# Kernel optimization log

Hardware: AMD Instinct MI355X
Metric: run time of the kernel (lower is better)

The kernel has to match this reference:

```python
import jax, jax.numpy as jnp
import numpy as np

TEMPERATURE = 8.0  # sqrt(head_dim=64)


def setup_inputs() -> dict:
    key = jax.random.key(0)
    ks = jax.random.split(key, 6)
    B, H, S, D = 8, 8, 1024, 64
    shp = (B, H, S, D)
    names = ["q_r", "q_i", "k_r", "k_i", "v_r", "v_i"]
    return {n: jax.random.normal(k, shp, dtype=jnp.float32) for n, k in zip(names, ks)}


def _mag_minmax_norm(attn):
    """cvnn.MagMinMaxNorm(dim=-1): min-max normalize the magnitude along the
    last axis while preserving phase: x * (|x| - min) / ((max - min) * |x|)."""
    mag = jnp.abs(attn)                              # [B,H,Sq,Sk] real
    mn = jnp.min(mag, axis=-1, keepdims=True)
    mx = jnp.max(mag, axis=-1, keepdims=True)
    return attn * ((mag - mn) / ((mx - mn) * mag))


def reference(q_r, q_i, k_r, k_i, v_r, v_i):
    q = jax.lax.complex(q_r, q_i)
    k = jax.lax.complex(k_r, k_i)
    v = jax.lax.complex(v_r, v_i)
    # complex QK^T with temperature scaling
    attn = jnp.einsum("bhqd,bhkd->bhqk", q / TEMPERATURE, k)
    attn = _mag_minmax_norm(attn)
    # dropout is identity at inference (eval mode)
    out = jnp.einsum("bhqk,bhkd->bhqd", attn, v)
    # return real/imag stacked: [2, B, H, S, D]
    return jnp.stack([out.real, out.imag])
```

## Files before the change

### kernel.cpp

```cpp
#include <hip/hip_runtime.h>
#include <math.h>

typedef unsigned short ushort_t;
typedef __attribute__((ext_vector_type(8))) short short8;
typedef __attribute__((ext_vector_type(4))) float f32x4;
typedef __attribute__((ext_vector_type(4))) int int4v;

constexpr int S = 1024, D = 64, BH = 64;
constexpr int HALF = BH * S * D;
constexpr int KROW = 72;
constexpr int VROW = 72;
constexpr int TILE_USH = 2 * 32 * KROW + 64 * VROW;
constexpr int TILE_B = TILE_USH * 2;
constexpr size_t WS_NEED = (size_t)BH * 32 * TILE_B;

#define MFMA16(a, b, c) __builtin_amdgcn_mfma_f32_16x16x32_bf16(a, b, c, 0, 0, 0)

__device__ __forceinline__ ushort_t f2bf(float f) {
  unsigned u = __float_as_uint(f);
  u += 0x7fff + ((u >> 16) & 1);
  return (ushort_t)(u >> 16);
}

__device__ __forceinline__ int4v pack8(float4 a, float4 b) {
  int4v r;
  r.x = (unsigned)f2bf(a.x) | ((unsigned)f2bf(a.y) << 16);
  r.y = (unsigned)f2bf(a.z) | ((unsigned)f2bf(a.w) << 16);
  r.z = (unsigned)f2bf(b.x) | ((unsigned)f2bf(b.y) << 16);
  r.w = (unsigned)f2bf(b.z) | ((unsigned)f2bf(b.w) << 16);
  return r;
}

#if defined(__has_builtin)
#if __has_builtin(__builtin_amdgcn_cvt_pk_bf16_f32)
#define HAS_CVT_PK_BF16 1
typedef __attribute__((ext_vector_type(2))) __bf16 bf16x2_t;
__device__ __forceinline__ unsigned cvtpk(float a, float b) {
  bf16x2_t v = __builtin_amdgcn_cvt_pk_bf16_f32(a, b);
  unsigned u;
  __builtin_memcpy(&u, &v, 4);
  return u;
}
#endif
#endif
#ifndef HAS_CVT_PK_BF16
#define HAS_CVT_PK_BF16 0
__device__ __forceinline__ unsigned cvtpk(float a, float b) {
  return (unsigned)f2bf(a) | ((unsigned)f2bf(b) << 16);
}
#endif

__device__ __forceinline__ short8 twist(short8 v) {
  int4v u;
  __builtin_memcpy(&u, &v, 16);
  int4v w;
  w.x = (int)((((unsigned)u.x >> 16) | ((unsigned)u.x << 16)) ^ 0x8000u);
  w.y = (int)((((unsigned)u.y >> 16) | ((unsigned)u.y << 16)) ^ 0x8000u);
  w.z = (int)((((unsigned)u.z >> 16) | ((unsigned)u.z << 16)) ^ 0x8000u);
  w.w = (int)((((unsigned)u.w >> 16) | ((unsigned)u.w << 16)) ^ 0x8000u);
  short8 r;
  __builtin_memcpy(&r, &w, 16);
  return r;
}

__global__ __launch_bounds__(256)
void prepass_kernel(const float* __restrict__ kr, const float* __restrict__ ki,
                    const float* __restrict__ vr, const float* __restrict__ vi,
                    ushort_t* __restrict__ ws) {
  __shared__ float svr[32 * 65], svi[32 * 65];
  const int t = threadIdx.x;
  const int tile = blockIdx.x;
  const size_t gbase = (size_t)tile * (32 * D);
  ushort_t* wst = ws + (size_t)tile * TILE_USH;
  const int k = t >> 3, d0 = (t & 7) * 8;
  const int dT = t >> 2, k0 = (t & 3) * 8;

  {
    float4 a = *(const float4*)(kr + gbase + k * D + d0);
    float4 b = *(const float4*)(kr + gbase + k * D + d0 + 4);
    *(int4v*)(wst + k * KROW + d0) = pack8(a, b);
  }
  {
    float4 a = *(const float4*)(ki + gbase + k * D + d0);
    float4 b = *(const float4*)(ki + gbase + k * D + d0 + 4);
    *(int4v*)(wst + 2304 + k * KROW + d0) = pack8(a, b);
  }
  {
    float4 a = *(const float4*)(vr + gbase + k * D + d0);
    float4 b = *(const float4*)(vr + gbase + k * D + d0 + 4);
    *(float4*)&svr[k * 65 + d0] = a;
    *(float4*)&svr[k * 65 + d0 + 4] = b;
    float4 c = *(const float4*)(vi + gbase + k * D + d0);
    float4 d = *(const float4*)(vi + gbase + k * D + d0 + 4);
    *(float4*)&svi[k * 65 + d0] = c;
    *(float4*)&svi[k * 65 + d0 + 4] = d;
  }
  __syncthreads();
  {
    unsigned dws[8];
#pragma unroll
    for (int j = 0; j < 8; ++j) {
      int s = k0 + j;
      dws[j] = cvtpk(svr[s * 65 + dT], -svi[s * 65 + dT]);
    }
    ushort_t* dst = wst + 4608 + dT * VROW + 2 * k0;
    *(int4v*)dst = *(int4v*)&dws[0];
    *(int4v*)(dst + 8) = *(int4v*)&dws[4];
  }
}

__global__ __launch_bounds__(256, 2)
void cvattn_mfma(const float* __restrict__ gq_r, const float* __restrict__ gq_i,
                 const ushort_t* __restrict__ ws, float* __restrict__ gout) {
  __shared__ __attribute__((aligned(16))) char smem[55296];
  ushort_t* sB = (ushort_t*)smem;
  const int t = threadIdx.x;
  const int lane = t & 63, wave = t >> 6;
  const int m = lane & 15, quad = lane >> 4;
  const int qt = blockIdx.x, bh = blockIdx.y;
  const size_t base = (size_t)bh * (S * D);

  unsigned* pwu = (unsigned*)(smem + 18432) + wave * 2304;

  short8 fQr[2][2], fQi[2][2];
#pragma unroll
  for (int h = 0; h < 2; ++h) {
    const int row = qt * 128 + h * 64 + wave * 16 + m;
#pragma unroll
    for (int dc = 0; dc < 2; ++dc) {
      const int d = dc * 32 + quad * 8;
      const float* pr = gq_r + base + (size_t)row * D + d;
      const float* pi = gq_i + base + (size_t)row * D + d;
      int4v vr_ = pack8(*(const float4*)pr, *(const float4*)(pr + 4));
      int4v vi_ = pack8(*(const float4*)pi, *(const float4*)(pi + 4));
      __builtin_memcpy(&fQr[h][dc], &vr_, 16);
      __builtin_memcpy(&fQi[h][dc], &vi_, 16);
    }
  }

  f32x4 aAr[2][4] = {}, aAi[2][4] = {}, aUr[2][4] = {}, aUi[2][4] = {};
  float mn4[2][4], mx4[2][4];
#pragma unroll
  for (int h = 0; h < 2; ++h)
#pragma unroll
    for (int r = 0; r < 4; ++r) { mn4[h][r] = 1e30f; mx4[h][r] = 0.f; }

  const ushort_t* wsrc = ws + (size_t)bh * 32 * TILE_USH;

  int4v pre[5];
#pragma unroll
  for (int i = 0; i < 5; ++i) {
    int idx = i * 256 + t;
    if (idx < TILE_B / 16) pre[i] = *(const int4v*)(wsrc + idx * 8);
  }

  for (int kb = 0; kb < 32; ++kb) {
    __syncthreads();
#pragma unroll
    for (int i = 0; i < 5; ++i) {
      int idx = i * 256 + t;
      if (idx < TILE_B / 16) *(int4v*)(smem + idx * 16) = pre[i];
    }
    if (kb + 1 < 32) {
      const ushort_t* g = wsrc + (size_t)(kb + 1) * TILE_USH;
#pragma unroll
      for (int i = 0; i < 5; ++i) {
        int idx = i * 256 + t;
        if (idx < TILE_B / 16) pre[i] = *(const int4v*)(g + idx * 8);
      }
    }
    __syncthreads();

#pragma unroll
    for (int ks = 0; ks < 2; ++ks) {
      const int krow = ks * 16 + m;
      short8 fKr0 = *(const short8*)&sB[krow * KROW + quad * 8];
      short8 fKr1 = *(const short8*)&sB[krow * KROW + 32 + quad * 8];
      short8 fKi0 = *(const short8*)&sB[2304 + krow * KROW + quad * 8];
      short8 fKi1 = *(const short8*)&sB[2304 + krow * KROW + 32 + quad * 8];
      short8 fKn0 = fKi0 ^ (short)0x8000;
      short8 fKn1 = fKi1 ^ (short)0x8000;
#pragma unroll
      for (int h = 0; h < 2; ++h) {
        f32x4 cSr = {}, cSi = {};
        cSr = MFMA16(fQr[h][0], fKr0, cSr);
        cSr = MFMA16(fQr[h][1], fKr1, cSr);
        cSr = MFMA16(fQi[h][0], fKn0, cSr);
        cSr = MFMA16(fQi[h][1], fKn1, cSr);
        cSi = MFMA16(fQr[h][0], fKi0, cSi);
        cSi = MFMA16(fQr[h][1], fKi1, cSi);
        cSi = MFMA16(fQi[h][0], fKr0, cSi);
        cSi = MFMA16(fQi[h][1], fKr1, cSi);
#pragma unroll
        for (int r = 0; r < 4; ++r) {
          float sr = cSr[r], si = cSi[r];
          float t2 = sr * sr + si * si;
          float rq = __builtin_amdgcn_rsqf(t2);
          mn4[h][r] = fminf(mn4[h][r], t2);
          mx4[h][r] = fmaxf(mx4[h][r], t2);
          const int dwo = h * 1152 + (quad * 4 + r) * 36 + ks * 16 + m;
          pwu[dwo] = cvtpk(sr, si);
          pwu[576 + dwo] = cvtpk(sr * rq, si * rq);
        }
      }
    }

    short8 fP0[2], fP1[2], fU0[2], fU1[2];
#pragma unroll
    for (int h = 0; h < 2; ++h) {
      const int bo = h * 1152 + m * 36 + quad * 4;
      fP0[h] = *(const short8*)&pwu[bo];
      fP1[h] = *(const short8*)&pwu[bo + 16];
      fU0[h] = *(const short8*)&pwu[576 + bo];
      fU1[h] = *(const short8*)&pwu[576 + bo + 16];
    }
#pragma unroll
    for (int dt = 0; dt < 4; ++dt) {
      const unsigned* vrow = (const unsigned*)sB + 2304 + (dt * 16 + m) * 36 + quad * 4;
      short8 vre0 = *(const short8*)vrow;
      short8 vre1 = *(const short8*)(vrow + 16);
      short8 vim0 = twist(vre0);
      short8 vim1 = twist(vre1);
#pragma unroll
      for (int h = 0; h < 2; ++h) {
        aAr[h][dt] = MFMA16(fP0[h], vre0, aAr[h][dt]);
        aAr[h][dt] = MFMA16(fP1[h], vre1, aAr[h][dt]);
        aAi[h][dt] = MFMA16(fP0[h], vim0, aAi[h][dt]);
        aAi[h][dt] = MFMA16(fP1[h], vim1, aAi[h][dt]);
        aUr[h][dt] = MFMA16(fU0[h], vre0, aUr[h][dt]);
        aUr[h][dt] = MFMA16(fU1[h], vre1, aUr[h][dt]);
        aUi[h][dt] = MFMA16(fU0[h], vim0, aUi[h][dt]);
        aUi[h][dt] = MFMA16(fU1[h], vim1, aUi[h][dt]);
      }
    }
  }

#pragma unroll
  for (int h = 0; h < 2; ++h) {
    float inv[4];
#pragma unroll
    for (int r = 0; r < 4; ++r) {
#pragma unroll
      for (int mask = 1; mask < 16; mask <<= 1) {
        mn4[h][r] = fminf(mn4[h][r], __shfl_xor(mn4[h][r], mask, 64));
        mx4[h][r] = fmaxf(mx4[h][r], __shfl_xor(mx4[h][r], mask, 64));
      }
      mn4[h][r] = sqrtf(mn4[h][r]);
      mx4[h][r] = sqrtf(mx4[h][r]);
      inv[r] = 1.0f / (mx4[h][r] - mn4[h][r]);
    }
    const int qbase = qt * 128 + h * 64 + wave * 16 + quad * 4;
#pragma unroll
    for (int dt = 0; dt < 4; ++dt) {
      const int d = dt * 16 + m;
#pragma unroll
      for (int r = 0; r < 4; ++r) {
        size_t o = base + (size_t)(qbase + r) * D + d;
        gout[o] = (aAr[h][dt][r] - mn4[h][r] * aUr[h][dt][r]) * inv[r];
        gout[HALF + o] = (aAi[h][dt][r] - mn4[h][r] * aUi[h][dt][r]) * inv[r];
      }
    }
  }
}

constexpr int QT = 32, KT = 32;
constexpr int DP = D + 4;
constexpr int KP = KT + 1;

#define CDOT4(SR, SI, AR, AI, BR, BI)                              \
  SR += AR.x*BR.x + AR.y*BR.y + AR.z*BR.z + AR.w*BR.w              \
      - AI.x*BI.x - AI.y*BI.y - AI.z*BI.z - AI.w*BI.w;             \
  SI += AR.x*BI.x + AR.y*BI.y + AR.z*BI.z + AR.w*BI.w              \
      + AI.x*BR.x + AI.y*BR.y + AI.z*BR.z + AI.w*BR.w;

__global__ __launch_bounds__(256, 2)
void cvattn_fallback(const float* __restrict__ gq_r, const float* __restrict__ gq_i,
                     const float* __restrict__ gk_r, const float* __restrict__ gk_i,
                     const float* __restrict__ gv_r, const float* __restrict__ gv_i,
                     float* __restrict__ gout) {
  __shared__ float qs_r[QT][DP], qs_i[QT][DP];
  __shared__ float ks_r[KT][DP], ks_i[KT][DP];
  __shared__ float vs_r[KT][DP], vs_i[KT][DP];
  __shared__ float sc_r[QT][KP], sc_i[QT][KP], sc_m[QT][KP];
  const int t = threadIdx.x;
  const int qt2 = blockIdx.x, bh = blockIdx.y;
  const size_t base = (size_t)bh * (S * D);
  {
    const float* qr_p = gq_r + base + (size_t)qt2 * QT * D;
    const float* qi_p = gq_i + base + (size_t)qt2 * QT * D;
#pragma unroll
    for (int i = 0; i < 2; ++i) {
      int e = (t + i * 256) * 4;
      int row = e >> 6, col = e & 63;
      *(float4*)&qs_r[row][col] = *(const float4*)(qr_p + e);
      *(float4*)&qs_i[row][col] = *(const float4*)(qi_p + e);
    }
  }
  const int q0 = (t >> 4) * 2, k0 = (t & 15) * 2;
  const int rB = t >> 3, dc = (t & 7) * 8;
  float Ar[8] = {}, Ai[8] = {}, Ur[8] = {}, Ui[8] = {};
  float mn = 3.4e38f, mx = 0.0f;
  for (int kb = 0; kb < S / KT; ++kb) {
    __syncthreads();
    {
      const float* kr_p = gk_r + base + (size_t)kb * KT * D;
      const float* ki_p = gk_i + base + (size_t)kb * KT * D;
      const float* vr_p = gv_r + base + (size_t)kb * KT * D;
      const float* vi_p = gv_i + base + (size_t)kb * KT * D;
#pragma unroll
      for (int i = 0; i < 2; ++i) {
        int e = (t + i * 256) * 4;
        int row = e >> 6, col = e & 63;
        *(float4*)&ks_r[row][col] = *(const float4*)(kr_p + e);
        *(float4*)&ks_i[row][col] = *(const float4*)(ki_p + e);
        *(float4*)&vs_r[row][col] = *(const float4*)(vr_p + e);
        *(float4*)&vs_i[row][col] = *(const float4*)(vi_p + e);
      }
    }
    __syncthreads();
    {
      float s00r=0.f,s00i=0.f,s01r=0.f,s01i=0.f;
      float s10r=0.f,s10i=0.f,s11r=0.f,s11i=0.f;
#pragma unroll
      for (int d = 0; d < D; d += 4) {
        float4 a0r = *(const float4*)&qs_r[q0  ][d];
        float4 a0i = *(const float4*)&qs_i[q0  ][d];
        float4 a1r = *(const float4*)&qs_r[q0+1][d];
        float4 a1i = *(const float4*)&qs_i[q0+1][d];
        float4 b0r = *(const float4*)&ks_r[k0  ][d];
        float4 b0i = *(const float4*)&ks_i[k0  ][d];
        float4 b1r = *(const float4*)&ks_r[k0+1][d];
        float4 b1i = *(const float4*)&ks_i[k0+1][d];
        CDOT4(s00r, s00i, a0r, a0i, b0r, b0i);
        CDOT4(s01r, s01i, a0r, a0i, b1r, b1i);
        CDOT4(s10r, s10i, a1r, a1i, b0r, b0i);
        CDOT4(s11r, s11i, a1r, a1i, b1r, b1i);
      }
      s00r *= 0.125f; s00i *= 0.125f; s01r *= 0.125f; s01i *= 0.125f;
      s10r *= 0.125f; s10i *= 0.125f; s11r *= 0.125f; s11i *= 0.125f;
      sc_r[q0  ][k0  ] = s00r; sc_i[q0  ][k0  ] = s00i;
      sc_m[q0  ][k0  ] = sqrtf(s00r*s00r + s00i*s00i);
      sc_r[q0  ][k0+1] = s01r; sc_i[q0  ][k0+1] = s01i;
      sc_m[q0  ][k0+1] = sqrtf(s01r*s01r + s01i*s01i);
      sc_r[q0+1][k0  ] = s10r; sc_i[q0+1][k0  ] = s10i;
      sc_m[q0+1][k0  ] = sqrtf(s10r*s10r + s10i*s10i);
      sc_r[q0+1][k0+1] = s11r; sc_i[q0+1][k0+1] = s11i;
      sc_m[q0+1][k0+1] = sqrtf(s11r*s11r + s11i*s11i);
    }
    __syncthreads();
#pragma unroll 8
    for (int k = 0; k < KT; ++k) {
      float sr = sc_r[rB][k], si = sc_i[rB][k], mg = sc_m[rB][k];
      mn = fminf(mn, mg); mx = fmaxf(mx, mg);
      float inv = 1.0f / mg;
      float ur = sr * inv, ui = si * inv;
      float vr[8], vi[8];
      *(float4*)&vr[0] = *(const float4*)&vs_r[k][dc];
      *(float4*)&vr[4] = *(const float4*)&vs_r[k][dc + 4];
      *(float4*)&vi[0] = *(const float4*)&vs_i[k][dc];
      *(float4*)&vi[4] = *(const float4*)&vs_i[k][dc + 4];
#pragma unroll
      for (int j = 0; j < 8; ++j) {
        Ar[j] += sr * vr[j] - si * vi[j];
        Ai[j] += sr * vi[j] + si * vr[j];
        Ur[j] += ur * vr[j] - ui * vi[j];
        Ui[j] += ur * vi[j] + ui * vr[j];
      }
    }
  }
  float invspan = 1.0f / (mx - mn);
  float outr[8], outi[8];
#pragma unroll
  for (int j = 0; j < 8; ++j) {
    outr[j] = (Ar[j] - mn * Ur[j]) * invspan;
    outi[j] = (Ai[j] - mn * Ui[j]) * invspan;
  }
  size_t o = base + (size_t)(qt2 * QT + rB) * D + dc;
  *(float4*)(gout + o)            = *(float4*)&outr[0];
  *(float4*)(gout + o + 4)        = *(float4*)&outr[4];
  *(float4*)(gout + HALF + o)     = *(float4*)&outi[0];
  *(float4*)(gout + HALF + o + 4) = *(float4*)&outi[4];
}

extern "C" void kernel_launch(void* const* d_in, const int* in_sizes, int n_in,
                              void* d_out, int out_size, void* d_ws, size_t ws_size,
                              hipStream_t stream) {
  if (ws_size >= WS_NEED) {
    prepass_kernel<<<dim3(BH * 32), 256, 0, stream>>>(
        (const float*)d_in[2], (const float*)d_in[3],
        (const float*)d_in[4], (const float*)d_in[5], (ushort_t*)d_ws);
    cvattn_mfma<<<dim3(S / 128, BH), 256, 0, stream>>>(
        (const float*)d_in[0], (const float*)d_in[1],
        (const ushort_t*)d_ws, (float*)d_out);
  } else {
    cvattn_fallback<<<dim3(S / QT, BH), 256, 0, stream>>>(
        (const float*)d_in[0], (const float*)d_in[1],
        (const float*)d_in[2], (const float*)d_in[3],
        (const float*)d_in[4], (const float*)d_in[5], (float*)d_out);
  }
}
```

Baseline: 256.3 us.

## Precompute twisted V tile in shared memory and remap block order

```diff
diff --git a/kernel.cpp b/kernel.cpp
--- a/kernel.cpp
+++ b/kernel.cpp
@@ -15,21 +15,6 @@
 constexpr size_t WS_NEED = (size_t)BH * 32 * TILE_B;
 
 #define MFMA16(a, b, c) __builtin_amdgcn_mfma_f32_16x16x32_bf16(a, b, c, 0, 0, 0)
-
-__device__ __forceinline__ ushort_t f2bf(float f) {
-  unsigned u = __float_as_uint(f);
-  u += 0x7fff + ((u >> 16) & 1);
-  return (ushort_t)(u >> 16);
-}
-
-__device__ __forceinline__ int4v pack8(float4 a, float4 b) {
-  int4v r;
-  r.x = (unsigned)f2bf(a.x) | ((unsigned)f2bf(a.y) << 16);
-  r.y = (unsigned)f2bf(a.z) | ((unsigned)f2bf(a.w) << 16);
-  r.z = (unsigned)f2bf(b.x) | ((unsigned)f2bf(b.y) << 16);
-  r.w = (unsigned)f2bf(b.z) | ((unsigned)f2bf(b.w) << 16);
-  return r;
-}
 
 #if defined(__has_builtin)
 #if __has_builtin(__builtin_amdgcn_cvt_pk_bf16_f32)
@@ -46,21 +31,30 @@
 #ifndef HAS_CVT_PK_BF16
 #define HAS_CVT_PK_BF16 0
 __device__ __forceinline__ unsigned cvtpk(float a, float b) {
-  return (unsigned)f2bf(a) | ((unsigned)f2bf(b) << 16);
+  __bf16 la = (__bf16)a, lb = (__bf16)b;
+  unsigned short lo, hi;
+  __builtin_memcpy(&lo, &la, 2);
+  __builtin_memcpy(&hi, &lb, 2);
+  return (unsigned)lo | ((unsigned)hi << 16);
 }
 #endif
 
-__device__ __forceinline__ short8 twist(short8 v) {
-  int4v u;
-  __builtin_memcpy(&u, &v, 16);
+__device__ __forceinline__ int4v pack8(float4 a, float4 b) {
+  int4v r;
+  r.x = (int)cvtpk(a.x, a.y);
+  r.y = (int)cvtpk(a.z, a.w);
+  r.z = (int)cvtpk(b.x, b.y);
+  r.w = (int)cvtpk(b.z, b.w);
+  return r;
+}
+
+__device__ __forceinline__ int4v twist4(int4v u) {
   int4v w;
   w.x = (int)((((unsigned)u.x >> 16) | ((unsigned)u.x << 16)) ^ 0x8000u);
   w.y = (int)((((unsigned)u.y >> 16) | ((unsigned)u.y << 16)) ^ 0x8000u);
   w.z = (int)((((unsigned)u.z >> 16) | ((unsigned)u.z << 16)) ^ 0x8000u);
   w.w = (int)((((unsigned)u.w >> 16) | ((unsigned)u.w << 16)) ^ 0x8000u);
-  short8 r;
-  __builtin_memcpy(&r, &w, 16);
-  return r;
+  return w;
 }
 
 __global__ __launch_bounds__(256)
@@ -112,15 +106,18 @@
 __global__ __launch_bounds__(256, 2)
 void cvattn_mfma(const float* __restrict__ gq_r, const float* __restrict__ gq_i,
                  const ushort_t* __restrict__ ws, float* __restrict__ gout) {
-  __shared__ __attribute__((aligned(16))) char smem[55296];
+  __shared__ __attribute__((aligned(16))) char smem[64512];
   ushort_t* sB = (ushort_t*)smem;
   const int t = threadIdx.x;
   const int lane = t & 63, wave = t >> 6;
   const int m = lane & 15, quad = lane >> 4;
-  const int qt = blockIdx.x, bh = blockIdx.y;
+
+  const int id = blockIdx.x;
+  const int bh = (id & 7) * 8 + ((id >> 3) & 7);
+  const int qt = id >> 6;
   const size_t base = (size_t)bh * (S * D);
 
-  unsigned* pwu = (unsigned*)(smem + 18432) + wave * 2304;
+  unsigned* pwu = (unsigned*)(smem + 27648) + wave * 2304;
 
   short8 fQr[2][2], fQi[2][2];
 #pragma unroll
@@ -159,7 +156,10 @@
 #pragma unroll
     for (int i = 0; i < 5; ++i) {
       int idx = i * 256 + t;
-      if (idx < TILE_B / 16) *(int4v*)(smem + idx * 16) = pre[i];
+      if (idx < TILE_B / 16) {
+        *(int4v*)(smem + idx * 16) = pre[i];
+        if (idx >= 576) *(int4v*)(smem + 18432 + (idx - 576) * 16) = twist4(pre[i]);
+      }
     }
     if (kb + 1 < 32) {
       const ushort_t* g = wsrc + (size_t)(kb + 1) * TILE_USH;
@@ -217,10 +217,11 @@
 #pragma unroll
     for (int dt = 0; dt < 4; ++dt) {
       const unsigned* vrow = (const unsigned*)sB + 2304 + (dt * 16 + m) * 36 + quad * 4;
+      const unsigned* virow = vrow + 2304;
       short8 vre0 = *(const short8*)vrow;
       short8 vre1 = *(const short8*)(vrow + 16);
-      short8 vim0 = twist(vre0);
-      short8 vim1 = twist(vre1);
+      short8 vim0 = *(const short8*)virow;
+      short8 vim1 = *(const short8*)(virow + 16);
 #pragma unroll
       for (int h = 0; h < 2; ++h) {
         aAr[h][dt] = MFMA16(fP0[h], vre0, aAr[h][dt]);
@@ -389,7 +390,7 @@
     prepass_kernel<<<dim3(BH * 32), 256, 0, stream>>>(
         (const float*)d_in[2], (const float*)d_in[3],
         (const float*)d_in[4], (const float*)d_in[5], (ushort_t*)d_ws);
-    cvattn_mfma<<<dim3(S / 128, BH), 256, 0, stream>>>(
+    cvattn_mfma<<<dim3(S / 128 * BH), 256, 0, stream>>>(
         (const float*)d_in[0], (const float*)d_in[1],
         (const ushort_t*)d_ws, (float*)d_out);
   } else {
```

New measurement: 248.4 us. 3.1% less time.
